# Kernel optimization log

Measured on AMD Instinct MI355X. Metric: run time of the kernel, lower is better.

## Reference

```python
import jax, jax.numpy as jnp
import numpy as np

D_MODEL = 256; N_HEADS = 8; N_LEVELS = 4; N_POINTS = 4; D_FFN = 1024
BS = 8; NQ = 100; NKPT = 17
LEVEL_SHAPES = [(160, 160), (80, 80), (40, 40), (20, 20)]  # (H, W) per level
LEN_V = sum(h * w for h, w in LEVEL_SHAPES)  # 34000


def layer_norm(x, g, b, eps=1e-5):
    m = x.mean(-1, keepdims=True)
    v = ((x - m) ** 2).mean(-1, keepdims=True)
    return (x - m) * jax.lax.rsqrt(v + eps) * g + b


def mha(q, k, v, Wqkv, bqkv, Wo, bo):
    # torch nn.MultiheadAttention, batch_first, eval mode (no dropout)
    d = q.shape[-1]; dh = d // N_HEADS
    def proj(x, W, b):
        return (x @ W.T + b).reshape(*x.shape[:-1], N_HEADS, dh)
    qp = proj(q, Wqkv[:d], bqkv[:d])
    kp = proj(k, Wqkv[d:2 * d], bqkv[d:2 * d])
    vp = proj(v, Wqkv[2 * d:], bqkv[2 * d:])
    att = jnp.einsum('bqhd,bkhd->bhqk', qp, kp) / jnp.sqrt(jnp.asarray(dh, q.dtype))
    att = jax.nn.softmax(att, -1)
    out = jnp.einsum('bhqk,bkhd->bqhd', att, vp).reshape(q.shape)
    return out @ Wo.T + bo


def bilinear_sample(val, loc, h, w):
    # val: (B, H, h*w, Dh); loc: (B, Lq, H, P, 2) normalized to [0,1]
    # matches F.grid_sample(align_corners=False, padding_mode='zeros') on grid 2*loc-1
    B, Lq, H, P, _ = loc.shape
    px = loc[..., 0] * w - 0.5
    py = loc[..., 1] * h - 0.5
    x0f = jnp.floor(px); y0f = jnp.floor(py)
    lx = px - x0f; ly = py - y0f
    x0 = x0f.astype(jnp.int32); y0 = y0f.astype(jnp.int32)
    out = jnp.zeros((B, H, Lq, P, val.shape[-1]), val.dtype)
    for dx, dy, wt in ((0, 0, (1 - lx) * (1 - ly)), (1, 0, lx * (1 - ly)),
                       (0, 1, (1 - lx) * ly), (1, 1, lx * ly)):
        xi = x0 + dx; yi = y0 + dy
        valid = ((xi >= 0) & (xi < w) & (yi >= 0) & (yi < h)).astype(val.dtype)
        idx = jnp.clip(yi, 0, h - 1) * w + jnp.clip(xi, 0, w - 1)  # (B,Lq,H,P)
        idx = idx.transpose(0, 2, 1, 3).reshape(B, H, Lq * P)
        g = jnp.take_along_axis(val, idx[..., None], axis=2).reshape(B, H, Lq, P, -1)
        out = out + g * (wt * valid).transpose(0, 2, 1, 3)[..., None]
    return out  # (B, H, Lq, P, Dh)


def ms_deform_attn(query, ref_points, memory, off_W, off_b, aw_W, aw_b,
                   val_W, val_b, outp_W, outp_b):
    B, Lq, _ = query.shape
    dh = D_MODEL // N_HEADS
    value = (memory @ val_W.T + val_b).reshape(B, LEN_V, N_HEADS, dh)
    off = (query @ off_W.T + off_b).reshape(B, Lq, N_HEADS, N_LEVELS, N_POINTS, 2)
    aw = (query @ aw_W.T + aw_b).reshape(B, Lq, N_HEADS, N_LEVELS * N_POINTS)
    aw = jax.nn.softmax(aw, -1).reshape(B, Lq, N_HEADS, N_LEVELS, N_POINTS)
    normalizer = jnp.array([[w, h] for h, w in LEVEL_SHAPES], dtype=query.dtype)  # (L,2) as (W,H)
    loc = ref_points[:, :, None, :, None, :] + off / normalizer[None, None, None, :, None, :]
    out = jnp.zeros((B, Lq, N_HEADS, dh), query.dtype)
    start = 0
    for l, (h, w) in enumerate(LEVEL_SHAPES):
        vl = value[:, start:start + h * w].transpose(0, 2, 1, 3)  # (B,H,hw,Dh)
        s = bilinear_sample(vl, loc[:, :, :, l], h, w)            # (B,H,Lq,P,Dh)
        out = out + jnp.einsum('bhqpd,bqhp->bqhd', s, aw[:, :, :, l])
        start += h * w
    return out.reshape(B, Lq, D_MODEL) @ outp_W.T + outp_b


def setup_inputs() -> dict:
    key = jax.random.key(0)
    ks = iter(jax.random.split(key, 40))
    d = D_MODEL
    def w(shape, s=0.02):
        return jax.random.normal(next(ks), shape, jnp.float32) * s
    inp = {
        'tgt_pose': jax.random.normal(next(ks), (BS, NQ, NKPT, d), jnp.float32),
        'tgt_pose_query_pos': jax.random.normal(next(ks), (BS, NQ, NKPT, d), jnp.float32),
        'tgt_pose_reference_points': jax.random.uniform(next(ks), (BS, NQ * NKPT, N_LEVELS, 2), jnp.float32),
        'memory': jax.random.normal(next(ks), (BS, LEN_V, d), jnp.float32),
        'win_Wqkv': w((3 * d, d)), 'win_bqkv': jnp.zeros((3 * d,), jnp.float32),
        'win_Wo': w((d, d)), 'win_bo': jnp.zeros((d,), jnp.float32),
        'win_ng': jnp.ones((d,), jnp.float32), 'win_nb': jnp.zeros((d,), jnp.float32),
        'acr_Wqkv': w((3 * d, d)), 'acr_bqkv': jnp.zeros((3 * d,), jnp.float32),
        'acr_Wo': w((d, d)), 'acr_bo': jnp.zeros((d,), jnp.float32),
        'acr_ng': jnp.ones((d,), jnp.float32), 'acr_nb': jnp.zeros((d,), jnp.float32),
        'off_W': w((N_HEADS * N_LEVELS * N_POINTS * 2, d)),
        'off_b': jax.random.uniform(next(ks), (N_HEADS * N_LEVELS * N_POINTS * 2,), jnp.float32, -1.0, 1.0),
        'aw_W': w((N_HEADS * N_LEVELS * N_POINTS, d)), 'aw_b': jnp.zeros((N_HEADS * N_LEVELS * N_POINTS,), jnp.float32),
        'val_W': w((d, d)), 'val_b': jnp.zeros((d,), jnp.float32),
        'outp_W': w((d, d)), 'outp_b': jnp.zeros((d,), jnp.float32),
        'gate_W': w((2 * d, 2 * d)), 'gate_b': jnp.zeros((2 * d,), jnp.float32),
        'gate_ng': jnp.ones((d,), jnp.float32), 'gate_nb': jnp.zeros((d,), jnp.float32),
        'ffn_W1': w((D_FFN, d)), 'ffn_b1': jnp.zeros((D_FFN,), jnp.float32),
        'ffn_W2': w((d, D_FFN)), 'ffn_b2': jnp.zeros((d,), jnp.float32),
        'n2_g': jnp.ones((d,), jnp.float32), 'n2_b': jnp.zeros((d,), jnp.float32),
        'memory_spatial_shapes': jnp.array(LEVEL_SHAPES, jnp.int32),
    }
    return inp


def reference(tgt_pose, tgt_pose_query_pos, tgt_pose_reference_points, memory,
              win_Wqkv, win_bqkv, win_Wo, win_bo, win_ng, win_nb,
              acr_Wqkv, acr_bqkv, acr_Wo, acr_bo, acr_ng, acr_nb,
              off_W, off_b, aw_W, aw_b, val_W, val_b, outp_W, outp_b,
              gate_W, gate_b, gate_ng, gate_nb,
              ffn_W1, ffn_b1, ffn_W2, ffn_b2, n2_g, n2_b,
              memory_spatial_shapes):
    bs, nq, K, d = tgt_pose.shape
    # with_pos_embed mutates tgt_pose in place in the torch code -> residual includes pos
    tgt = tgt_pose + tgt_pose_query_pos
    # within-attention over keypoints of each query
    x = tgt.reshape(bs * nq, K, d)
    t2 = mha(x, x, x, win_Wqkv, win_bqkv, win_Wo, win_bo).reshape(bs, nq, K, d)
    tgt = layer_norm(tgt + t2, win_ng, win_nb)
    # across-attention over queries for each keypoint
    xk = tgt.transpose(0, 2, 1, 3).reshape(bs * K, nq, d)
    t2 = mha(xk, xk, xk, acr_Wqkv, acr_bqkv, acr_Wo, acr_bo)
    tgt = layer_norm(xk + t2, acr_ng, acr_nb).reshape(bs, K, nq, d).transpose(0, 2, 1, 3)
    # second in-place pos add before deformable cross-attn (also feeds gateway)
    tgt_q = tgt + tgt_pose_query_pos
    t2 = ms_deform_attn(tgt_q.reshape(bs, nq * K, d), tgt_pose_reference_points, memory,
                        off_W, off_b, aw_W, aw_b, val_W, val_b, outp_W, outp_b)
    t2 = t2.reshape(bs, nq, K, d)
    # Gate
    g = jax.nn.sigmoid(jnp.concatenate([tgt_q, t2], -1) @ gate_W.T + gate_b)
    g1, g2 = jnp.split(g, 2, -1)
    tgt = layer_norm(g1 * tgt_q + g2 * t2, gate_ng, gate_nb)
    # FFN
    h = jax.nn.relu(tgt @ ffn_W1.T + ffn_b1)
    tgt = tgt + h @ ffn_W2.T + ffn_b2
    tgt = layer_norm(jnp.clip(tgt, -65504.0, 65504.0), n2_g, n2_b)
    return tgt
```

## Files before the change

### kernel.cpp

```cpp
#include <hip/hip_runtime.h>
#include <hip/hip_bf16.h>

#define NH 8
#define BS_ 8
#define NQ_ 100
#define NK_ 17
#define LQ 1700
#define T_TOK 13600
#define LEN_VV 34000

typedef __attribute__((ext_vector_type(8))) short short8v;
typedef __attribute__((ext_vector_type(8))) __bf16 bf16x8;
typedef __attribute__((ext_vector_type(4))) float f32x4;

__device__ __forceinline__ short f2bf(float f){
  __hip_bfloat16 h = __float2bfloat16(f);
  return *reinterpret_cast<short*>(&h);
}
__device__ __forceinline__ float bf2f(short s){
  return __uint_as_float(((uint)(unsigned short)s) << 16);
}
__device__ __forceinline__ short8v cvt8(float4 a, float4 b){
  short8v u;
  u[0]=f2bf(a.x); u[1]=f2bf(a.y); u[2]=f2bf(a.z); u[3]=f2bf(a.w);
  u[4]=f2bf(b.x); u[5]=f2bf(b.y); u[6]=f2bf(b.z); u[7]=f2bf(b.w);
  return u;
}

__global__ __launch_bounds__(256, 4) void mgemm_k(const float* __restrict__ A,
                                                  const float* __restrict__ W,
                                                  const float* __restrict__ bias,
                                                  __hip_bfloat16* __restrict__ Cb,
                                                  int M, int N, int K, int nbx){
  __shared__ short sh[128 * 136];
  short* As = sh;
  short* Ws = sh + 128 * 64;
  int total = gridDim.x;
  int q = total >> 3, r = total & 7;
  int x = blockIdx.x & 7, k = blockIdx.x >> 3;
  int j = (x < r) ? x * (q + 1) + k : r * (q + 1) + (x - r) * q + k;
  const int tid = threadIdx.x;
  const int bm = (j / nbx) * 128, bn = (j % nbx) * 128;
  const int wave = tid >> 6, lane = tid & 63;
  const int wm = (wave >> 1) * 64, wn = (wave & 1) * 64;
  const int s = tid & 7;
  const int row0 = tid >> 3;
  f32x4 acc[4][4] = {};
  const int lrow = lane & 15, lk = lane >> 4;

  for (int k0 = 0; k0 < K; k0 += 64){
#pragma unroll
    for (int i = 0; i < 4; i++){
      int row = row0 + i * 32;
      int gr = bm + row;
      int sw = ((s ^ (row & 7)) << 3) + row * 64;
      short8v va = {};
      if (gr < M){
        const float* p = A + (size_t)gr * K + k0 + s * 8;
        va = cvt8(((const float4*)p)[0], ((const float4*)p)[1]);
      }
      *(short8v*)&As[sw] = va;
      const float* q2 = W + (size_t)(bn + row) * K + k0 + s * 8;
      *(short8v*)&Ws[sw] = cvt8(((const float4*)q2)[0], ((const float4*)q2)[1]);
    }
    __syncthreads();
#pragma unroll
    for (int ks = 0; ks < 2; ks++){
      short8v af[4], bw[4];
      int slot = ks * 4 + lk;
#pragma unroll
      for (int m = 0; m < 4; m++){
        int rr = wm + m * 16 + lrow;
        af[m] = *(const short8v*)&As[rr * 64 + ((slot ^ (rr & 7)) << 3)];
      }
#pragma unroll
      for (int n = 0; n < 4; n++){
        int rr = wn + n * 16 + lrow;
        bw[n] = *(const short8v*)&Ws[rr * 64 + ((slot ^ (rr & 7)) << 3)];
      }
#pragma unroll
      for (int m = 0; m < 4; m++)
#pragma unroll
        for (int n = 0; n < 4; n++)
          acc[m][n] = __builtin_amdgcn_mfma_f32_16x16x32_bf16(
              __builtin_bit_cast(bf16x8, af[m]),
              __builtin_bit_cast(bf16x8, bw[n]), acc[m][n], 0, 0, 0);
    }
    __syncthreads();
  }
  const int STR = 136;
#pragma unroll
  for (int n = 0; n < 4; n++){
    int col = wn + n * 16 + lrow;
    float bsv = bias[bn + col];
#pragma unroll
    for (int m = 0; m < 4; m++){
#pragma unroll
      for (int i = 0; i < 4; i++){
        int row = wm + m * 16 + lk * 4 + i;
        sh[row * STR + col] = f2bf(acc[m][n][i] + bsv);
      }
    }
  }
  __syncthreads();
#pragma unroll
  for (int it = 0; it < 8; it++){
    int rr = it * 16 + (tid >> 4);
    int chunk = tid & 15;
    if (bm + rr < M){
      uint4 v = *(const uint4*)((const char*)sh + rr * 272 + chunk * 16);
      *(uint4*)((char*)Cb + ((size_t)(bm + rr) * N + bn) * 2 + chunk * 16) = v;
    }
  }
}

template<int EPI, int ADDA, int INB>
__global__ __launch_bounds__(256) void mgemmP_k(const void* __restrict__ Av,
                                                const float* __restrict__ A2,
                                                const float* __restrict__ W,
                                                const float* __restrict__ bias,
                                                __hip_bfloat16* __restrict__ Cb,
                                                int M, int N, int K, int nbx){
  __shared__ short sh[128 * 136];
  short* As = sh;
  short* Ws = sh + 128 * 64;
  const float* A = (const float*)Av;
  const short* Ab = (const short*)Av;
  const int tid = threadIdx.x;
  const int j = blockIdx.x;
  const int bm = (j / nbx) * 128, bn = (j % nbx) * 128;
  const int wave = tid >> 6, lane = tid & 63;
  const int wm = (wave >> 1) * 64, wn = (wave & 1) * 64;
  const int s = tid & 7;
  const int row0 = tid >> 3;
  f32x4 acc[4][4] = {};
  const int lrow = lane & 15, lk = lane >> 4;

  float4 ra[INB ? 1 : 8], rw[8];
  short8v rab[INB ? 4 : 1];
#pragma unroll
  for (int i = 0; i < 4; i++){
    int row = row0 + i * 32;
    int gr = bm + row;
    if (INB){
      short8v z = {};
      rab[INB ? i : 0] = (gr < M) ? *(const short8v*)(Ab + (size_t)gr * K + s * 8) : z;
    } else {
      float4 z = make_float4(0.f, 0.f, 0.f, 0.f);
      if (gr < M){
        const float* p = A + (size_t)gr * K + s * 8;
        float4 x0 = ((const float4*)p)[0], x1 = ((const float4*)p)[1];
        if (ADDA){
          const float* q2 = A2 + (size_t)gr * K + s * 8;
          float4 y0 = ((const float4*)q2)[0], y1 = ((const float4*)q2)[1];
          x0.x+=y0.x; x0.y+=y0.y; x0.z+=y0.z; x0.w+=y0.w;
          x1.x+=y1.x; x1.y+=y1.y; x1.z+=y1.z; x1.w+=y1.w;
        }
        ra[INB ? 0 : (2 * i)] = x0; ra[INB ? 0 : (2 * i + 1)] = x1;
      } else { ra[INB ? 0 : (2 * i)] = z; ra[INB ? 0 : (2 * i + 1)] = z; }
    }
    const float* q = W + (size_t)(bn + row) * K + s * 8;
    rw[2 * i] = ((const float4*)q)[0]; rw[2 * i + 1] = ((const float4*)q)[1];
  }

  for (int k0 = 0; k0 < K; k0 += 64){
#pragma unroll
    for (int i = 0; i < 4; i++){
      int row = row0 + i * 32;
      int sw = ((s ^ (row & 7)) << 3) + row * 64;
      if (INB) *(short8v*)&As[sw] = rab[INB ? i : 0];
      else     *(short8v*)&As[sw] = cvt8(ra[INB ? 0 : (2 * i)], ra[INB ? 0 : (2 * i + 1)]);
      *(short8v*)&Ws[sw] = cvt8(rw[2 * i], rw[2 * i + 1]);
    }
    __syncthreads();
    if (k0 + 64 < K){
#pragma unroll
      for (int i = 0; i < 4; i++){
        int row = row0 + i * 32;
        int gr = bm + row;
        if (INB){
          short8v z = {};
          rab[INB ? i : 0] = (gr < M) ? *(const short8v*)(Ab + (size_t)gr * K + k0 + 64 + s * 8) : z;
        } else {
          float4 z = make_float4(0.f, 0.f, 0.f, 0.f);
          if (gr < M){
            const float* p = A + (size_t)gr * K + k0 + 64 + s * 8;
            float4 x0 = ((const float4*)p)[0], x1 = ((const float4*)p)[1];
            if (ADDA){
              const float* q2 = A2 + (size_t)gr * K + k0 + 64 + s * 8;
              float4 y0 = ((const float4*)q2)[0], y1 = ((const float4*)q2)[1];
              x0.x+=y0.x; x0.y+=y0.y; x0.z+=y0.z; x0.w+=y0.w;
              x1.x+=y1.x; x1.y+=y1.y; x1.z+=y1.z; x1.w+=y1.w;
            }
            ra[INB ? 0 : (2 * i)] = x0; ra[INB ? 0 : (2 * i + 1)] = x1;
          } else { ra[INB ? 0 : (2 * i)] = z; ra[INB ? 0 : (2 * i + 1)] = z; }
        }
        const float* q = W + (size_t)(bn + row) * K + k0 + 64 + s * 8;
        rw[2 * i] = ((const float4*)q)[0]; rw[2 * i + 1] = ((const float4*)q)[1];
      }
    }
#pragma unroll
    for (int ks = 0; ks < 2; ks++){
      short8v af[4], bw[4];
      int slot = ks * 4 + lk;
#pragma unroll
      for (int m = 0; m < 4; m++){
        int rr = wm + m * 16 + lrow;
        af[m] = *(const short8v*)&As[rr * 64 + ((slot ^ (rr & 7)) << 3)];
      }
#pragma unroll
      for (int n = 0; n < 4; n++){
        int rr = wn + n * 16 + lrow;
        bw[n] = *(const short8v*)&Ws[rr * 64 + ((slot ^ (rr & 7)) << 3)];
      }
#pragma unroll
      for (int m = 0; m < 4; m++)
#pragma unroll
        for (int n = 0; n < 4; n++)
          acc[m][n] = __builtin_amdgcn_mfma_f32_16x16x32_bf16(
              __builtin_bit_cast(bf16x8, af[m]),
              __builtin_bit_cast(bf16x8, bw[n]), acc[m][n], 0, 0, 0);
    }
    __syncthreads();
  }
  const int STR = 136;
#pragma unroll
  for (int n = 0; n < 4; n++){
    int col = wn + n * 16 + lrow;
    float bsv = bias[bn + col];
#pragma unroll
    for (int m = 0; m < 4; m++){
#pragma unroll
      for (int i = 0; i < 4; i++){
        int row = wm + m * 16 + lk * 4 + i;
        float c = acc[m][n][i] + bsv;
        if (EPI == 1) c = fmaxf(c, 0.f);
        sh[row * STR + col] = f2bf(c);
      }
    }
  }
  __syncthreads();
#pragma unroll
  for (int it = 0; it < 8; it++){
    int rr = it * 16 + (tid >> 4);
    int chunk = tid & 15;
    if (bm + rr < M){
      uint4 v = *(const uint4*)((const char*)sh + rr * 272 + chunk * 16);
      *(uint4*)((char*)Cb + ((size_t)(bm + rr) * N + bn) * 2 + chunk * 16) = v;
    }
  }
}

template<int SITE, int OUTB>
__global__ __launch_bounds__(256) void gln_k(const short* __restrict__ Abf,
                                             const float* __restrict__ W,
                                             const float* __restrict__ bias,
                                             const float* __restrict__ r0,
                                             const float* __restrict__ r1,
                                             const float* __restrict__ g,
                                             const float* __restrict__ be,
                                             void* __restrict__ outv,
                                             int M, int K){
  __shared__ short As[32 * 64];
  __shared__ short Ws[256 * 64];
  __shared__ float part[32][4][2];
  __shared__ float stats[32][2];
  const int tid = threadIdx.x;
  const int bm = blockIdx.x * 32;
  const int wave = tid >> 6, lane = tid & 63;
  const int wn = wave * 64;
  const int s = tid & 7, row0 = tid >> 3;
  const int lrow = lane & 15, lk = lane >> 4;
  f32x4 acc[2][4] = {};

  short8v pa = {};
  { int gr = bm + row0; if (gr < M) pa = *(const short8v*)(Abf + (size_t)gr * K + s * 8); }
  short8v pwb[8];
#pragma unroll
  for (int i = 0; i < 8; i++){
    const float* wp = W + (size_t)(row0 + i * 32) * K + s * 8;
    pwb[i] = cvt8(((const float4*)wp)[0], ((const float4*)wp)[1]);
  }

  for (int k0 = 0; k0 < K; k0 += 64){
    *(short8v*)&As[row0 * 64 + ((s ^ (row0 & 7)) << 3)] = pa;
#pragma unroll
    for (int i = 0; i < 8; i++){
      int row = row0 + i * 32;
      *(short8v*)&Ws[row * 64 + ((s ^ (row & 7)) << 3)] = pwb[i];
    }
    __syncthreads();
    if (k0 + 64 < K){
      int gr = bm + row0;
      pa = (short8v){};
      if (gr < M) pa = *(const short8v*)(Abf + (size_t)gr * K + k0 + 64 + s * 8);
#pragma unroll
      for (int i = 0; i < 8; i++){
        const float* wp = W + (size_t)(row0 + i * 32) * K + k0 + 64 + s * 8;
        pwb[i] = cvt8(((const float4*)wp)[0], ((const float4*)wp)[1]);
      }
    }
#pragma unroll
    for (int ks = 0; ks < 2; ks++){
      int slot = ks * 4 + lk;
      short8v af[2], bw[4];
#pragma unroll
      for (int m = 0; m < 2; m++){
        int rr = m * 16 + lrow;
        af[m] = *(const short8v*)&As[rr * 64 + ((slot ^ (rr & 7)) << 3)];
      }
#pragma unroll
      for (int n = 0; n < 4; n++){
        int rr = wn + n * 16 + lrow;
        bw[n] = *(const short8v*)&Ws[rr * 64 + ((slot ^ (rr & 7)) << 3)];
      }
#pragma unroll
      for (int m = 0; m < 2; m++)
#pragma unroll
        for (int n = 0; n < 4; n++)
          acc[m][n] = __builtin_amdgcn_mfma_f32_16x16x32_bf16(
              __builtin_bit_cast(bf16x8, af[m]),
              __builtin_bit_cast(bf16x8, bw[n]), acc[m][n], 0, 0, 0);
    }
    __syncthreads();
  }

#pragma unroll
  for (int m = 0; m < 2; m++){
#pragma unroll
    for (int i = 0; i < 4; i++){
      int row = m * 16 + lk * 4 + i;
      int grow = bm + row;
      float s1 = 0.f, s2 = 0.f;
      if (grow < M){
#pragma unroll
        for (int n = 0; n < 4; n++){
          int col = wn + n * 16 + lrow;
          float x = acc[m][n][i] + bias[col] + r0[(size_t)grow * 256 + col];
          if (SITE == 0) x += r1[(size_t)grow * 256 + col];
          if (SITE == 2) x = fminf(fmaxf(x, -65504.f), 65504.f);
          acc[m][n][i] = x;
          s1 += x; s2 += x * x;
        }
      }
#pragma unroll
      for (int msk = 1; msk <= 8; msk <<= 1){
        s1 += __shfl_xor(s1, msk, 64);
        s2 += __shfl_xor(s2, msk, 64);
      }
      if (lrow == 0){ part[row][wave][0] = s1; part[row][wave][1] = s2; }
    }
  }
  __syncthreads();
  if (tid < 32){
    float s1 = part[tid][0][0] + part[tid][1][0] + part[tid][2][0] + part[tid][3][0];
    float s2 = part[tid][0][1] + part[tid][1][1] + part[tid][2][1] + part[tid][3][1];
    float mean = s1 * (1.f / 256.f);
    float var = s2 * (1.f / 256.f) - mean * mean;
    stats[tid][0] = mean;
    stats[tid][1] = rsqrtf(fmaxf(var, 0.f) + 1e-5f);
  }
  __syncthreads();
#pragma unroll
  for (int m = 0; m < 2; m++){
#pragma unroll
    for (int i = 0; i < 4; i++){
      int row = m * 16 + lk * 4 + i;
      int grow = bm + row;
      if (grow >= M) continue;
      float mean = stats[row][0], rstd = stats[row][1];
      size_t orow = grow;
      if (SITE == 0){
        int bi = grow / LQ; int rem = grow % LQ; int qq = rem / NK_; int kk = rem % NK_;
        orow = (size_t)bi * LQ + kk * NQ_ + qq;
      }
#pragma unroll
      for (int n = 0; n < 4; n++){
        int col = wn + n * 16 + lrow;
        float o = (acc[m][n][i] - mean) * rstd * g[col] + be[col];
        if (OUTB) ((short*)outv)[orow * 256 + col] = f2bf(o);
        else      ((float*)outv)[orow * 256 + col] = o;
      }
    }
  }
}

__global__ __launch_bounds__(256) void glnoa_k(const short* __restrict__ Abf,
                                               const float* __restrict__ W,
                                               const float* __restrict__ bias,
                                               const short* __restrict__ r0b,
                                               const float* __restrict__ qpos,
                                               const float* __restrict__ g,
                                               const float* __restrict__ be,
                                               short* __restrict__ TQout,
                                               float* __restrict__ OFFAW,
                                               const float* __restrict__ off_W,
                                               const float* __restrict__ aw_W,
                                               const float* __restrict__ off_b,
                                               const float* __restrict__ aw_b,
                                               int M){
  __shared__ short smem[32 * 256 + 384 * 64];
  __shared__ float part[32][4][2];
  __shared__ float stats[32][2];
  short* As1 = smem;
  short* Ws1 = smem + 32 * 64;
  short* As2 = smem;
  short* Ws2 = smem + 32 * 256;
  const int K = 256;
  const int tid = threadIdx.x;
  const int bm = blockIdx.x * 32;
  const int wave = tid >> 6, lane = tid & 63;
  const int wn = wave * 64;
  const int s = tid & 7, row0 = tid >> 3;
  const int lrow = lane & 15, lk = lane >> 4;
  f32x4 acc[2][4] = {};

  short8v pa = {};
  { int gr = bm + row0; if (gr < M) pa = *(const short8v*)(Abf + (size_t)gr * K + s * 8); }
  short8v pwb[8];
#pragma unroll
  for (int i = 0; i < 8; i++){
    const float* wp = W + (size_t)(row0 + i * 32) * K + s * 8;
    pwb[i] = cvt8(((const float4*)wp)[0], ((const float4*)wp)[1]);
  }
  for (int k0 = 0; k0 < K; k0 += 64){
    *(short8v*)&As1[row0 * 64 + ((s ^ (row0 & 7)) << 3)] = pa;
#pragma unroll
    for (int i = 0; i < 8; i++){
      int row = row0 + i * 32;
      *(short8v*)&Ws1[row * 64 + ((s ^ (row & 7)) << 3)] = pwb[i];
    }
    __syncthreads();
    if (k0 + 64 < K){
      int gr = bm + row0;
      pa = (short8v){};
      if (gr < M) pa = *(const short8v*)(Abf + (size_t)gr * K + k0 + 64 + s * 8);
#pragma unroll
      for (int i = 0; i < 8; i++){
        const float* wp = W + (size_t)(row0 + i * 32) * K + k0 + 64 + s * 8;
        pwb[i] = cvt8(((const float4*)wp)[0], ((const float4*)wp)[1]);
      }
    }
#pragma unroll
    for (int ks = 0; ks < 2; ks++){
      int slot = ks * 4 + lk;
      short8v af[2], bw[4];
#pragma unroll
      for (int m = 0; m < 2; m++){
        int rr = m * 16 + lrow;
        af[m] = *(const short8v*)&As1[rr * 64 + ((slot ^ (rr & 7)) << 3)];
      }
#pragma unroll
      for (int n = 0; n < 4; n++){
        int rr = wn + n * 16 + lrow;
        bw[n] = *(const short8v*)&Ws1[rr * 64 + ((slot ^ (rr & 7)) << 3)];
      }
#pragma unroll
      for (int m = 0; m < 2; m++)
#pragma unroll
        for (int n = 0; n < 4; n++)
          acc[m][n] = __builtin_amdgcn_mfma_f32_16x16x32_bf16(
              __builtin_bit_cast(bf16x8, af[m]),
              __builtin_bit_cast(bf16x8, bw[n]), acc[m][n], 0, 0, 0);
    }
    __syncthreads();
  }
#pragma unroll
  for (int m = 0; m < 2; m++){
#pragma unroll
    for (int i = 0; i < 4; i++){
      int row = m * 16 + lk * 4 + i;
      int grow = bm + row;
      float s1 = 0.f, s2 = 0.f;
      if (grow < M){
#pragma unroll
        for (int n = 0; n < 4; n++){
          int col = wn + n * 16 + lrow;
          float x = acc[m][n][i] + bias[col] + bf2f(r0b[(size_t)grow * 256 + col]);
          acc[m][n][i] = x;
          s1 += x; s2 += x * x;
        }
      }
#pragma unroll
      for (int msk = 1; msk <= 8; msk <<= 1){
        s1 += __shfl_xor(s1, msk, 64);
        s2 += __shfl_xor(s2, msk, 64);
      }
      if (lrow == 0){ part[row][wave][0] = s1; part[row][wave][1] = s2; }
    }
  }
  __syncthreads();
  if (tid < 32){
    float s1 = part[tid][0][0] + part[tid][1][0] + part[tid][2][0] + part[tid][3][0];
    float s2 = part[tid][0][1] + part[tid][1][1] + part[tid][2][1] + part[tid][3][1];
    float mean = s1 * (1.f / 256.f);
    float var = s2 * (1.f / 256.f) - mean * mean;
    stats[tid][0] = mean;
    stats[tid][1] = rsqrtf(fmaxf(var, 0.f) + 1e-5f);
  }
  __syncthreads();
#pragma unroll
  for (int m = 0; m < 2; m++){
#pragma unroll
    for (int i = 0; i < 4; i++){
      int row = m * 16 + lk * 4 + i;
      int grow = bm + row;
      float mean = stats[row][0], rstd = stats[row][1];
      size_t orow = 0;
      if (grow < M){
        int bi = grow / LQ; int rem = grow % LQ; int kk = rem / NQ_; int qq = rem % NQ_;
        orow = (size_t)bi * LQ + qq * NK_ + kk;
      }
#pragma unroll
      for (int n = 0; n < 4; n++){
        int col = wn + n * 16 + lrow;
        float tq = 0.f;
        if (grow < M){
          float o = (acc[m][n][i] - mean) * rstd * g[col] + be[col];
          tq = o + qpos[orow * 256 + col];
          TQout[orow * 256 + col] = f2bf(tq);
        }
        As2[row * 256 + ((((col >> 3) ^ (row & 7)) << 3) + (col & 7))] = f2bf(tq);
      }
    }
  }
  __syncthreads();
  const int wn2 = wave * 96;
  f32x4 acc2[2][6] = {};
  for (int k0 = 0; k0 < 256; k0 += 64){
#pragma unroll
    for (int it = 0; it < 12; it++){
      int wr = row0 + it * 32;
      const float* Wp = (wr < 256) ? off_W + (size_t)wr * 256 + k0
                                   : aw_W + (size_t)(wr - 256) * 256 + k0;
      *(short8v*)&Ws2[wr * 64 + ((s ^ (wr & 7)) << 3)] =
          cvt8(((const float4*)(Wp + s * 8))[0], ((const float4*)(Wp + s * 8))[1]);
    }
    __syncthreads();
#pragma unroll
    for (int ks = 0; ks < 2; ks++){
      int slotl = ks * 4 + lk;
      int slotg = (k0 >> 3) + slotl;
      short8v af[2], bw[6];
#pragma unroll
      for (int m = 0; m < 2; m++){
        int rr = m * 16 + lrow;
        af[m] = *(const short8v*)&As2[rr * 256 + ((slotg ^ (rr & 7)) << 3)];
      }
#pragma unroll
      for (int n = 0; n < 6; n++){
        int rr = wn2 + n * 16 + lrow;
        bw[n] = *(const short8v*)&Ws2[rr * 64 + ((slotl ^ (rr & 7)) << 3)];
      }
#pragma unroll
      for (int m = 0; m < 2; m++)
#pragma unroll
        for (int n = 0; n < 6; n++)
          acc2[m][n] = __builtin_amdgcn_mfma_f32_16x16x32_bf16(
              __builtin_bit_cast(bf16x8, af[m]),
              __builtin_bit_cast(bf16x8, bw[n]), acc2[m][n], 0, 0, 0);
    }
    __syncthreads();
  }
#pragma unroll
  for (int m = 0; m < 2; m++){
#pragma unroll
    for (int i = 0; i < 4; i++){
      int row = m * 16 + lk * 4 + i;
      int grow = bm + row;
      if (grow >= M) continue;
      int bi = grow / LQ; int rem = grow % LQ; int kk = rem / NQ_; int qq = rem % NQ_;
      size_t orow = (size_t)bi * LQ + qq * NK_ + kk;
#pragma unroll
      for (int n = 0; n < 6; n++){
        int col = wn2 + n * 16 + lrow;
        float c = acc2[m][n][i] + ((col < 256) ? off_b[col] : aw_b[col - 256]);
        OFFAW[orow * 384 + col] = c;
      }
    }
  }
}

__global__ __launch_bounds__(256) void t2gateln_k(const short* __restrict__ ABF,
                                                  const float* __restrict__ outp_W,
                                                  const float* __restrict__ outp_b,
                                                  const short* __restrict__ TQ,
                                                  const float* __restrict__ gW,
                                                  const float* __restrict__ gbias,
                                                  const float* __restrict__ g,
                                                  const float* __restrict__ be,
                                                  float* __restrict__ out, int M){
  __shared__ short As[32 * 64];
  __shared__ short T2s[32 * 256];
  __shared__ short Ws[512 * 64];
  const int tid = threadIdx.x;
  const int bm = blockIdx.x * 32;
  const int wave = tid >> 6, lane = tid & 63;
  const int s = tid & 7, row0 = tid >> 3;
  const int lrow = lane & 15, lk = lane >> 4;

  {
    const int wn = wave * 64;
    f32x4 acc[2][4] = {};
    for (int k0 = 0; k0 < 256; k0 += 64){
      {
        short8v v = {};
        int gr = bm + row0;
        if (gr < M) v = *(const short8v*)(ABF + (size_t)gr * 256 + k0 + s * 8);
        *(short8v*)&As[row0 * 64 + ((s ^ (row0 & 7)) << 3)] = v;
      }
#pragma unroll
      for (int i = 0; i < 8; i++){
        int row = row0 + i * 32;
        const float* wp = outp_W + (size_t)row * 256 + k0 + s * 8;
        *(short8v*)&Ws[row * 64 + ((s ^ (row & 7)) << 3)] =
            cvt8(((const float4*)wp)[0], ((const float4*)wp)[1]);
      }
      __syncthreads();
#pragma unroll
      for (int ks = 0; ks < 2; ks++){
        int slot = ks * 4 + lk;
        short8v af[2], bw[4];
#pragma unroll
        for (int m = 0; m < 2; m++){
          int rr = m * 16 + lrow;
          af[m] = *(const short8v*)&As[rr * 64 + ((slot ^ (rr & 7)) << 3)];
        }
#pragma unroll
        for (int n = 0; n < 4; n++){
          int rr = wn + n * 16 + lrow;
          bw[n] = *(const short8v*)&Ws[rr * 64 + ((slot ^ (rr & 7)) << 3)];
        }
#pragma unroll
        for (int m = 0; m < 2; m++)
#pragma unroll
          for (int n = 0; n < 4; n++)
            acc[m][n] = __builtin_amdgcn_mfma_f32_16x16x32_bf16(
                __builtin_bit_cast(bf16x8, af[m]),
                __builtin_bit_cast(bf16x8, bw[n]), acc[m][n], 0, 0, 0);
      }
      __syncthreads();
    }
#pragma unroll
    for (int m = 0; m < 2; m++){
#pragma unroll
      for (int i = 0; i < 4; i++){
        int row = m * 16 + lk * 4 + i;
#pragma unroll
        for (int n = 0; n < 4; n++){
          int col = wn + n * 16 + lrow;
          float t2v = acc[m][n][i] + outp_b[col];
          T2s[row * 256 + ((((col >> 3) ^ (row & 7)) << 3) + (col & 7))] = f2bf(t2v);
        }
      }
    }
  }
  __syncthreads();

  const int wn = wave * 128;
  f32x4 acc[2][8] = {};
  for (int kt = 0; kt < 8; kt++){
    int k0 = kt * 64;
    if (kt < 4){
      short8v v = {};
      int gr = bm + row0;
      if (gr < M) v = *(const short8v*)(TQ + (size_t)gr * 256 + k0 + s * 8);
      *(short8v*)&As[row0 * 64 + ((s ^ (row0 & 7)) << 3)] = v;
    }
#pragma unroll
    for (int i = 0; i < 16; i++){
      int row = row0 + i * 32;
      const float* wp = gW + (size_t)row * 512 + k0 + s * 8;
      *(short8v*)&Ws[row * 64 + ((s ^ (row & 7)) << 3)] =
          cvt8(((const float4*)wp)[0], ((const float4*)wp)[1]);
    }
    __syncthreads();
#pragma unroll
    for (int ks = 0; ks < 2; ks++){
      int slot = ks * 4 + lk;
      short8v af[2], bw[8];
#pragma unroll
      for (int m = 0; m < 2; m++){
        int rr = m * 16 + lrow;
        if (kt < 4){
          af[m] = *(const short8v*)&As[rr * 64 + ((slot ^ (rr & 7)) << 3)];
        } else {
          int slotg = ((k0 - 256) >> 3) + slot;
          af[m] = *(const short8v*)&T2s[rr * 256 + ((slotg ^ (rr & 7)) << 3)];
        }
      }
#pragma unroll
      for (int n = 0; n < 8; n++){
        int rr = wn + n * 16 + lrow;
        bw[n] = *(const short8v*)&Ws[rr * 64 + ((slot ^ (rr & 7)) << 3)];
      }
#pragma unroll
      for (int m = 0; m < 2; m++)
#pragma unroll
        for (int n = 0; n < 8; n++)
          acc[m][n] = __builtin_amdgcn_mfma_f32_16x16x32_bf16(
              __builtin_bit_cast(bf16x8, af[m]),
              __builtin_bit_cast(bf16x8, bw[n]), acc[m][n], 0, 0, 0);
    }
    __syncthreads();
  }
  short* gb = Ws;
  const int GSTR = 520;
#pragma unroll
  for (int n = 0; n < 8; n++){
    int col = wn + n * 16 + lrow;
    float bsv = gbias[col];
#pragma unroll
    for (int m = 0; m < 2; m++){
#pragma unroll
      for (int i = 0; i < 4; i++){
        int row = m * 16 + lk * 4 + i;
        float c = acc[m][n][i] + bsv;
        gb[row * GSTR + col] = f2bf(1.f / (1.f + __expf(-c)));
      }
    }
  }
  __syncthreads();
  {
    int row = tid >> 3, cg = tid & 7;
    int grow = bm + row;
    float x[32];
    float s1 = 0.f, s2 = 0.f;
    if (grow < M){
#pragma unroll
      for (int jv = 0; jv < 4; jv++){
        int c0 = cg * 32 + jv * 8;
        short8v aqv = *(const short8v*)(TQ + (size_t)grow * 256 + c0);
        int slot2 = (cg * 4 + jv) ^ (row & 7);
        const short* t2p = &T2s[row * 256 + slot2 * 8];
#pragma unroll
        for (int jj = 0; jj < 8; jj++){
          float g1 = bf2f(gb[row * GSTR + c0 + jj]);
          float g2 = bf2f(gb[row * GSTR + 256 + c0 + jj]);
          float xv = g1 * bf2f(aqv[jj]) + g2 * bf2f(t2p[jj]);
          x[jv * 8 + jj] = xv; s1 += xv; s2 += xv * xv;
        }
      }
    }
    s1 += __shfl_xor(s1, 1, 64); s2 += __shfl_xor(s2, 1, 64);
    s1 += __shfl_xor(s1, 2, 64); s2 += __shfl_xor(s2, 2, 64);
    s1 += __shfl_xor(s1, 4, 64); s2 += __shfl_xor(s2, 4, 64);
    float mean = s1 * (1.f / 256.f);
    float var = s2 * (1.f / 256.f) - mean * mean;
    float rstd = rsqrtf(fmaxf(var, 0.f) + 1e-5f);
    if (grow < M){
#pragma unroll
      for (int jv = 0; jv < 4; jv++){
        int c0 = cg * 32 + jv * 8;
        float4 o0, o1;
#pragma unroll
        for (int jj = 0; jj < 8; jj++){
          int c = c0 + jj;
          float o = (x[jv * 8 + jj] - mean) * rstd * g[c] + be[c];
          if (jj < 4) ((float*)&o0)[jj] = o; else ((float*)&o1)[jj - 4] = o;
        }
        *(float4*)(out + (size_t)grow * 256 + c0) = o0;
        *(float4*)(out + (size_t)grow * 256 + c0 + 4) = o1;
      }
    }
  }
}

template<int TP, int NSPL>
__global__ __launch_bounds__(256) void mha_mfma_k(const short* __restrict__ qkv,
                                                  __hip_bfloat16* __restrict__ out, int S){
  constexpr int MT = TP / 16;
  constexpr int KSTEPS = (TP + 31) / 32;
  constexpr int KS32 = KSTEPS * 32;
  constexpr int VSTRB = (KS32 == 128) ? 256 : 128;
  constexpr int CH = (MT + NSPL - 1) / NSPL;
  __shared__ short QK[2][TP][64];
  __shared__ short Vt[2][32][VSTRB / 2];
  __shared__ float Sc[2][16][128];
  __shared__ float rinv[2][16];

  const int tid = threadIdx.x;
  const int bid = blockIdx.x;
  const int batch = bid / (4 * NSPL);
  const int rem = bid % (4 * NSPL);
  const int hp = rem / NSPL;
  const int half = rem % NSPL;
  const int mtlo = half * CH;
  const int mthi = (mtlo + CH < MT) ? (mtlo + CH) : MT;
  const int wave = tid >> 6, lane = tid & 63;
  const int hh = wave >> 1, wsub = wave & 1;
  const int lrow = lane & 15, lk = lane >> 4;
  const float scale = 0.17677669529663687f;
  const size_t qbase = (size_t)batch * S * 768;

  for (int idx = tid; idx < 2 * TP * 4; idx += 256){
    int h2 = idx >= TP * 4;
    int rm = idx - h2 * TP * 4;
    int j = rm >> 2, s = rm & 3;
    int h = hp * 2 + h2;
    short8v qv = {}, kv = {};
    if (j < S){
      const short* p = qkv + qbase + (size_t)j * 768 + h * 32 + s * 8;
      qv = *(const short8v*)p;
      kv = *(const short8v*)(p + 256);
    }
    *(short8v*)&QK[h2][j][(s ^ (j & 7)) << 3] = qv;
    *(short8v*)&QK[h2][j][((s + 4) ^ (j & 7)) << 3] = kv;
  }
  for (int idx = tid; idx < 2 * KS32 * 4; idx += 256){
    int h2 = idx >= KS32 * 4;
    int rm = idx - h2 * KS32 * 4;
    int j = rm >> 2, e8 = rm & 3;
    int h = hp * 2 + h2;
    short8v v = {};
    if (j < S) v = *(const short8v*)(qkv + qbase + (size_t)j * 768 + h * 32 + 512 + e8 * 8);
#pragma unroll
    for (int c = 0; c < 8; c++){
      int e = e8 * 8 + c;
      char* pb = (char*)&Vt[h2][0][0] + e * VSTRB + (((j >> 3) ^ (e & 7)) << 4) + ((j & 7) << 1);
      *(short*)pb = v[c];
    }
  }
  __syncthreads();

  for (int mt = mtlo; mt < mthi; mt++){
    for (int nt = wsub; nt < MT; nt += 2){
      int ar = mt * 16 + lrow;
      short8v aq = *(const short8v*)&QK[hh][ar][(lk ^ (ar & 7)) << 3];
      int br = nt * 16 + lrow;
      short8v bk = *(const short8v*)&QK[hh][br][((lk + 4) ^ (br & 7)) << 3];
      f32x4 z = {};
      f32x4 d = __builtin_amdgcn_mfma_f32_16x16x32_bf16(
          __builtin_bit_cast(bf16x8, aq), __builtin_bit_cast(bf16x8, bk), z, 0, 0, 0);
#pragma unroll
      for (int i = 0; i < 4; i++){
        int rr = lk * 4 + i;
        int c = nt * 16 + lrow;
        Sc[hh][rr][(((c >> 2) ^ (rr & 7)) << 2) + (c & 3)] = d[i] * scale;
      }
    }
    __syncthreads();
    if (wsub == 0){
      int rr = lane >> 2, p = lane & 3;
      int grow = mt * 16 + rr;
      int Seff = (grow < S) ? S : 0;
      float mx = -1e30f;
#pragma unroll
      for (int m = 0; m < KSTEPS; m++){
        int j = p + 4 * m;
#pragma unroll
        for (int hf = 0; hf < 2; hf++){
          int ls = 2 * j + hf;
          float4 v = *(const float4*)&Sc[hh][rr][(ls ^ (rr & 7)) << 2];
          int c0 = ls * 4;
          mx = fmaxf(mx, (c0 + 0 < Seff) ? v.x : -1e30f);
          mx = fmaxf(mx, (c0 + 1 < Seff) ? v.y : -1e30f);
          mx = fmaxf(mx, (c0 + 2 < Seff) ? v.z : -1e30f);
          mx = fmaxf(mx, (c0 + 3 < Seff) ? v.w : -1e30f);
        }
      }
      mx = fmaxf(mx, __shfl_xor(mx, 1, 64));
      mx = fmaxf(mx, __shfl_xor(mx, 2, 64));
      float sum = 0.f;
#pragma unroll
      for (int m = 0; m < KSTEPS; m++){
        int j = p + 4 * m;
        float ev[8];
#pragma unroll
        for (int hf = 0; hf < 2; hf++){
          int ls = 2 * j + hf;
          float4 v = *(const float4*)&Sc[hh][rr][(ls ^ (rr & 7)) << 2];
          int c0 = ls * 4;
          ev[hf * 4 + 0] = (c0 + 0 < Seff) ? __expf(v.x - mx) : 0.f;
          ev[hf * 4 + 1] = (c0 + 1 < Seff) ? __expf(v.y - mx) : 0.f;
          ev[hf * 4 + 2] = (c0 + 2 < Seff) ? __expf(v.z - mx) : 0.f;
          ev[hf * 4 + 3] = (c0 + 3 < Seff) ? __expf(v.w - mx) : 0.f;
        }
        short8v pb;
#pragma unroll
        for (int q2 = 0; q2 < 8; q2++){ pb[q2] = f2bf(ev[q2]); sum += ev[q2]; }
        *(short8v*)((char*)&Sc[hh][rr][0] + ((j ^ (rr & 7)) << 4)) = pb;
      }
      sum += __shfl_xor(sum, 1, 64);
      sum += __shfl_xor(sum, 2, 64);
      if (p == 0) rinv[hh][rr] = (sum > 0.f) ? 1.f / sum : 0.f;
    }
    __syncthreads();
    {
      int nt2 = wsub;
      f32x4 acc = {};
#pragma unroll
      for (int ks = 0; ks < KSTEPS; ks++){
        int slot = ks * 4 + lk;
        short8v ap = *(const short8v*)((const char*)&Sc[hh][lrow][0] + ((slot ^ (lrow & 7)) << 4));
        int e = nt2 * 16 + lrow;
        short8v bv = *(const short8v*)((const char*)&Vt[hh][0][0] + e * VSTRB + ((slot ^ (e & 7)) << 4));
        acc = __builtin_amdgcn_mfma_f32_16x16x32_bf16(
            __builtin_bit_cast(bf16x8, ap), __builtin_bit_cast(bf16x8, bv), acc, 0, 0, 0);
      }
      int h = hp * 2 + hh;
#pragma unroll
      for (int i = 0; i < 4; i++){
        int row = mt * 16 + lk * 4 + i;
        if (row < S){
          float rv = rinv[hh][lk * 4 + i];
          out[((size_t)batch * S + row) * 256 + h * 32 + nt2 * 16 + lrow] =
              __float2bfloat16(acc[i] * rv);
        }
      }
    }
    __syncthreads();
  }
}

__global__ __launch_bounds__(256) void deform_k(const __hip_bfloat16* __restrict__ val,
                                                const float* __restrict__ offaw,
                                                const float* __restrict__ ref,
                                                unsigned int* __restrict__ outb){
  __shared__ uint2 meta[32][16][4];
  const int tid = threadIdx.x;
  const int t0 = blockIdx.x * 4;
  {
    int g = tid >> 3;
    int pair = tid & 7;
    int lt = g >> 3, h = g & 7;
    int t = t0 + lt;
    int b = t / LQ;
    int p0 = pair * 2;
    int l = p0 >> 2;
    const int starts[4] = {0, 25600, 32000, 33600};
    const int HS[4] = {160, 80, 40, 20};
    int w = HS[l];
    const float* ap = offaw + (size_t)t * 384 + 256 + h * 16;
    float a0 = ap[p0];
    float a1 = ap[p0 + 1];
    float mx = fmaxf(a0, a1);
#pragma unroll
    for (int m = 1; m <= 4; m <<= 1) mx = fmaxf(mx, __shfl_xor(mx, m, 64));
    float e0 = expf(a0 - mx), e1 = expf(a1 - mx);
    float s = e0 + e1;
#pragma unroll
    for (int m = 1; m <= 4; m <<= 1) s += __shfl_xor(s, m, 64);
    float inv = 1.f / s;
    float rx = ref[((size_t)t * 4 + l) * 2 + 0];
    float ry = ref[((size_t)t * 4 + l) * 2 + 1];
    float4 ov = *(const float4*)(offaw + (size_t)t * 384 + h * 32 + l * 8 + p0 * 2);
    int vbase = (b * LEN_VV + starts[l]) * 128 + h * 16;
#pragma unroll
    for (int pp = 0; pp < 2; pp++){
      float wgt = (pp ? e1 : e0) * inv;
      float px = rx * w + (pp ? ov.z : ov.x) - 0.5f;
      float py = ry * w + (pp ? ov.w : ov.y) - 0.5f;
      float x0f = floorf(px), y0f = floorf(py);
      float lx = px - x0f, ly = py - y0f;
      int x0 = (int)x0f, y0 = (int)y0f;
#pragma unroll
      for (int c = 0; c < 4; c++){
        int dx = c & 1, dy = c >> 1;
        int xi = x0 + dx, yi = y0 + dy;
        bool ok = (xi >= 0) & (xi < w) & (yi >= 0) & (yi < w);
        float cw = ok ? wgt * (dx ? lx : 1.f - lx) * (dy ? ly : 1.f - ly) : 0.f;
        uint idx = ok ? (uint)(vbase + (yi * w + xi) * 128) : 0u;
        uint2 m2; m2.x = idx; m2.y = __float_as_uint(cw);
        meta[g][p0 + pp][c] = m2;
      }
    }
  }
  __syncthreads();
  const uint2* V2 = (const uint2*)val;
  int sg = tid >> 3, lane8 = tid & 7;
  int lt = sg >> 3, h = sg & 7;
  int t = t0 + lt;
  float a0 = 0.f, a1 = 0.f, a2 = 0.f, a3 = 0.f;
#pragma unroll 4
  for (int c = 0; c < 64; c++){
    uint2 mw = meta[sg][c >> 2][c & 3];
    float wv = __uint_as_float(mw.y);
    uint2 v = V2[(size_t)(mw.x >> 1) + lane8];
    a0 += wv * __uint_as_float(v.x << 16);
    a1 += wv * __uint_as_float(v.x & 0xffff0000u);
    a2 += wv * __uint_as_float(v.y << 16);
    a3 += wv * __uint_as_float(v.y & 0xffff0000u);
  }
  uint2 u;
  u.x = ((uint)(unsigned short)f2bf(a1) << 16) | (uint)(unsigned short)f2bf(a0);
  u.y = ((uint)(unsigned short)f2bf(a3) << 16) | (uint)(unsigned short)f2bf(a2);
  ((uint2*)outb)[((size_t)t * 256 + h * 32) / 4 + lane8] = u;
}

extern "C" void kernel_launch(void* const* d_in, const int* in_sizes, int n_in,
                              void* d_out, int out_size, void* d_ws, size_t ws_size,
                              hipStream_t stream){
  const float* tgt_pose = (const float*)d_in[0];
  const float* qpos     = (const float*)d_in[1];
  const float* refp     = (const float*)d_in[2];
  const float* memory   = (const float*)d_in[3];
  const float* win_Wqkv = (const float*)d_in[4];
  const float* win_bqkv = (const float*)d_in[5];
  const float* win_Wo   = (const float*)d_in[6];
  const float* win_bo   = (const float*)d_in[7];
  const float* win_ng   = (const float*)d_in[8];
  const float* win_nb   = (const float*)d_in[9];
  const float* acr_Wqkv = (const float*)d_in[10];
  const float* acr_bqkv = (const float*)d_in[11];
  const float* acr_Wo   = (const float*)d_in[12];
  const float* acr_bo   = (const float*)d_in[13];
  const float* acr_ng   = (const float*)d_in[14];
  const float* acr_nb   = (const float*)d_in[15];
  const float* off_W    = (const float*)d_in[16];
  const float* off_b    = (const float*)d_in[17];
  const float* aw_W     = (const float*)d_in[18];
  const float* aw_b     = (const float*)d_in[19];
  const float* val_W    = (const float*)d_in[20];
  const float* val_b    = (const float*)d_in[21];
  const float* outp_W   = (const float*)d_in[22];
  const float* outp_b   = (const float*)d_in[23];
  const float* gate_W   = (const float*)d_in[24];
  const float* gate_b   = (const float*)d_in[25];
  const float* gate_ng  = (const float*)d_in[26];
  const float* gate_nb  = (const float*)d_in[27];
  const float* ffn_W1   = (const float*)d_in[28];
  const float* ffn_b1   = (const float*)d_in[29];
  const float* ffn_W2   = (const float*)d_in[30];
  const float* ffn_b2   = (const float*)d_in[31];
  const float* n2_g     = (const float*)d_in[32];
  const float* n2_b     = (const float*)d_in[33];

  float* out = (float*)d_out;
  char* ws = (char*)d_ws;
  const size_t TB = (size_t)T_TOK * 256 * 4;
  float* B2 = (float*)(ws);
  char* p = ws + TB;
  short* B1b = (short*)p;  p += (size_t)T_TOK * 256 * 2;
  short* Qb  = (short*)p;  p += (size_t)T_TOK * 768 * 2;
  short* ABF = (short*)p;  p += (size_t)T_TOK * 256 * 2;
  short* TQb = (short*)p;  p += (size_t)T_TOK * 256 * 2;
  float* OFFAW = (float*)p; p += (size_t)T_TOK * 384 * 4;
  char* Vregion = p;
  __hip_bfloat16* V = (__hip_bfloat16*)Vregion;
  short* FF = (short*)Vregion;

  const int GM128 = (T_TOK + 127) / 128;
  const int GM32  = (T_TOK + 31) / 32;

  mgemm_k<<<2 * 2125, 256, 0, stream>>>(memory, val_W, val_b, V, BS_ * LEN_VV, 256, 256, 2);
  mgemmP_k<0,1,0><<<6 * GM128, 256, 0, stream>>>(tgt_pose, qpos, win_Wqkv, win_bqkv, (__hip_bfloat16*)Qb, T_TOK, 768, 256, 6);
  mha_mfma_k<32,1><<<800 * 4, 256, 0, stream>>>(Qb, (__hip_bfloat16*)ABF, 17);
  gln_k<0,1><<<GM32, 256, 0, stream>>>(ABF, win_Wo, win_bo, tgt_pose, qpos, win_ng, win_nb, B1b, T_TOK, 256);
  mgemmP_k<0,0,1><<<6 * GM128, 256, 0, stream>>>(B1b, nullptr, acr_Wqkv, acr_bqkv, (__hip_bfloat16*)Qb, T_TOK, 768, 256, 6);
  mha_mfma_k<112,2><<<136 * 8, 256, 0, stream>>>(Qb, (__hip_bfloat16*)ABF, 100);
  glnoa_k<<<GM32, 256, 0, stream>>>(ABF, acr_Wo, acr_bo, B1b, qpos, acr_ng, acr_nb,
                                    TQb, OFFAW, off_W, aw_W, off_b, aw_b, T_TOK);
  deform_k<<<T_TOK / 4, 256, 0, stream>>>(V, OFFAW, refp, (unsigned int*)ABF);
  t2gateln_k<<<GM32, 256, 0, stream>>>(ABF, outp_W, outp_b, TQb, gate_W, gate_b,
                                       gate_ng, gate_nb, B2, T_TOK);
  mgemmP_k<1,0,0><<<8 * GM128, 256, 0, stream>>>(B2, nullptr, ffn_W1, ffn_b1, (__hip_bfloat16*)FF, T_TOK, 1024, 256, 8);
  gln_k<2,0><<<GM32, 256, 0, stream>>>(FF, ffn_W2, ffn_b2, B2, nullptr, n2_g, n2_b, out, T_TOK, 1024);
}
```

Baseline: 477.8 us.

## Split fused output-proj/gate kernel into separate 64x64 GEMM and gate-LN kernels

The fused t2gateln kernel, which computed the deformable-attention output projection in shared memory before the gate GEMM and layernorm, is split in two. A new generic 64x64-tile bf16 MFMA GEMM kernel writes the projected t2 to a new bf16 workspace buffer, and a slimmer gate+layernorm kernel reads TQ and T2 from global memory. The fused kernel used a lot of LDS per block, which limits occupancy; the split lowers that footprint and gives the projection a better-shaped grid. The cost is an extra launch plus a global write and read of the t2 intermediate.

Result: faster. 462.7 us (-3.2%).

```diff
diff --git a/kernel.cpp b/kernel.cpp
--- a/kernel.cpp
+++ b/kernel.cpp
@@ -247,6 +247,129 @@
     if (bm + rr < M){
       uint4 v = *(const uint4*)((const char*)sh + rr * 272 + chunk * 16);
       *(uint4*)((char*)Cb + ((size_t)(bm + rr) * N + bn) * 2 + chunk * 16) = v;
+    }
+  }
+}
+
+template<int EPI, int OUTB, int INB, int DUALA>
+__global__ __launch_bounds__(256) void g64_k(const void* __restrict__ Av,
+                                             const void* __restrict__ A1v,
+                                             const float* __restrict__ W0,
+                                             const float* __restrict__ W1,
+                                             int NSPLIT,
+                                             const float* __restrict__ bias0,
+                                             const float* __restrict__ bias1,
+                                             const float* __restrict__ RES,
+                                             float* __restrict__ Cf,
+                                             __hip_bfloat16* __restrict__ Cb,
+                                             int M, int N, int K, int sA){
+  __shared__ short sh64[2 * 64 * 64];
+  short* As = sh64;
+  short* Ws = sh64 + 64 * 64;
+  const int tid = threadIdx.x;
+  const int bn = blockIdx.x * 64, bm = blockIdx.y * 64;
+  const int wave = tid >> 6, lane = tid & 63;
+  const int wm = (wave >> 1) * 32, wn = (wave & 1) * 32;
+  const int s = tid & 7, row0 = tid >> 3;
+  const int lrow = lane & 15, lk = lane >> 4;
+  f32x4 acc[2][2] = {};
+
+  for (int k0 = 0; k0 < K; k0 += 64){
+#pragma unroll
+    for (int i = 0; i < 2; i++){
+      int row = row0 + i * 32;
+      int sw = ((s ^ (row & 7)) << 3) + row * 64;
+      short8v v = {};
+      int gr = bm + row;
+      if (gr < M){
+        if (INB){
+          v = *(const short8v*)((const short*)Av + (size_t)gr * sA + k0 + s * 8);
+        } else {
+          const float* Ap;
+          if (DUALA) Ap = (k0 < 256) ? (const float*)Av + (size_t)gr * 256 + k0
+                                     : (const float*)A1v + (size_t)gr * 256 + (k0 - 256);
+          else Ap = (const float*)Av + (size_t)gr * sA + k0;
+          v = cvt8(((const float4*)(Ap + s * 8))[0], ((const float4*)(Ap + s * 8))[1]);
+        }
+      }
+      *(short8v*)&As[sw] = v;
+      int wr = bn + row;
+      const float* Wp = (wr < NSPLIT) ? W0 + (size_t)wr * K + k0
+                                      : W1 + (size_t)(wr - NSPLIT) * K + k0;
+      *(short8v*)&Ws[sw] = cvt8(((const float4*)(Wp + s * 8))[0], ((const float4*)(Wp + s * 8))[1]);
+    }
+    __syncthreads();
+#pragma unroll
+    for (int ks = 0; ks < 2; ks++){
+      int slot = ks * 4 + lk;
+      short8v af[2], bw[2];
+#pragma unroll
+      for (int m = 0; m < 2; m++){
+        int rr = wm + m * 16 + lrow;
+        af[m] = *(const short8v*)&As[rr * 64 + ((slot ^ (rr & 7)) << 3)];
+      }
+#pragma unroll
+      for (int n = 0; n < 2; n++){
+        int rr = wn + n * 16 + lrow;
+        bw[n] = *(const short8v*)&Ws[rr * 64 + ((slot ^ (rr & 7)) << 3)];
+      }
+#pragma unroll
+      for (int m = 0; m < 2; m++)
+#pragma unroll
+        for (int n = 0; n < 2; n++)
+          acc[m][n] = __builtin_amdgcn_mfma_f32_16x16x32_bf16(
+              __builtin_bit_cast(bf16x8, af[m]),
+              __builtin_bit_cast(bf16x8, bw[n]), acc[m][n], 0, 0, 0);
+    }
+    __syncthreads();
+  }
+  if (OUTB){
+    const int STR = 72;
+#pragma unroll
+    for (int n = 0; n < 2; n++){
+      int col = wn + n * 16 + lrow;
+      int gc = bn + col;
+      float bsv = (gc < NSPLIT) ? bias0[gc] : bias1[gc - NSPLIT];
+#pragma unroll
+      for (int m = 0; m < 2; m++){
+#pragma unroll
+        for (int i = 0; i < 4; i++){
+          int row = wm + m * 16 + lk * 4 + i;
+          float c = acc[m][n][i] + bsv;
+          if (EPI == 1) c = fmaxf(c, 0.f);
+          if (EPI == 2) c = 1.f / (1.f + expf(-c));
+          sh64[row * STR + col] = f2bf(c);
+        }
+      }
+    }
+    __syncthreads();
+#pragma unroll
+    for (int it = 0; it < 2; it++){
+      int rr = it * 32 + (tid >> 3);
+      int chunk = tid & 7;
+      if (bm + rr < M){
+        uint4 v = *(const uint4*)((const char*)sh64 + rr * 144 + chunk * 16);
+        *(uint4*)((char*)Cb + ((size_t)(bm + rr) * N + bn) * 2 + chunk * 16) = v;
+      }
+    }
+  } else {
+#pragma unroll
+    for (int n = 0; n < 2; n++){
+      int gc = bn + wn + n * 16 + lrow;
+      float bsv = (gc < NSPLIT) ? bias0[gc] : bias1[gc - NSPLIT];
+#pragma unroll
+      for (int m = 0; m < 2; m++){
+#pragma unroll
+        for (int i = 0; i < 4; i++){
+          int row = bm + wm + m * 16 + lk * 4 + i;
+          if (row >= M) continue;
+          float c = acc[m][n][i] + bsv;
+          if (EPI == 1) c = fmaxf(c, 0.f);
+          if (EPI == 2) c = 1.f / (1.f + expf(-c));
+          if (EPI == 3) c += RES[(size_t)row * N + gc];
+          Cf[(size_t)row * N + gc] = c;
+        }
+      }
     }
   }
 }
@@ -581,96 +704,38 @@
   }
 }
 
-__global__ __launch_bounds__(256) void t2gateln_k(const short* __restrict__ ABF,
-                                                  const float* __restrict__ outp_W,
-                                                  const float* __restrict__ outp_b,
-                                                  const short* __restrict__ TQ,
-                                                  const float* __restrict__ gW,
-                                                  const float* __restrict__ gbias,
-                                                  const float* __restrict__ g,
-                                                  const float* __restrict__ be,
-                                                  float* __restrict__ out, int M){
-  __shared__ short As[32 * 64];
-  __shared__ short T2s[32 * 256];
-  __shared__ short Ws[512 * 64];
+__global__ __launch_bounds__(256) void gateln_k(const short* __restrict__ TQ,
+                                                const short* __restrict__ T2,
+                                                const float* __restrict__ W,
+                                                const float* __restrict__ bias,
+                                                const float* __restrict__ g,
+                                                const float* __restrict__ be,
+                                                float* __restrict__ out, int M){
+  __shared__ short sh[32 * 64 + 512 * 64];
+  short* As = sh;
+  short* Ws = sh + 32 * 64;
   const int tid = threadIdx.x;
   const int bm = blockIdx.x * 32;
   const int wave = tid >> 6, lane = tid & 63;
+  const int wn = wave * 128;
   const int s = tid & 7, row0 = tid >> 3;
   const int lrow = lane & 15, lk = lane >> 4;
-
-  {
-    const int wn = wave * 64;
-    f32x4 acc[2][4] = {};
-    for (int k0 = 0; k0 < 256; k0 += 64){
-      {
-        short8v v = {};
-        int gr = bm + row0;
-        if (gr < M) v = *(const short8v*)(ABF + (size_t)gr * 256 + k0 + s * 8);
-        *(short8v*)&As[row0 * 64 + ((s ^ (row0 & 7)) << 3)] = v;
-      }
-#pragma unroll
-      for (int i = 0; i < 8; i++){
-        int row = row0 + i * 32;
-        const float* wp = outp_W + (size_t)row * 256 + k0 + s * 8;
-        *(short8v*)&Ws[row * 64 + ((s ^ (row & 7)) << 3)] =
-            cvt8(((const float4*)wp)[0], ((const float4*)wp)[1]);
-      }
-      __syncthreads();
-#pragma unroll
-      for (int ks = 0; ks < 2; ks++){
-        int slot = ks * 4 + lk;
-        short8v af[2], bw[4];
-#pragma unroll
-        for (int m = 0; m < 2; m++){
-          int rr = m * 16 + lrow;
-          af[m] = *(const short8v*)&As[rr * 64 + ((slot ^ (rr & 7)) << 3)];
-        }
-#pragma unroll
-        for (int n = 0; n < 4; n++){
-          int rr = wn + n * 16 + lrow;
-          bw[n] = *(const short8v*)&Ws[rr * 64 + ((slot ^ (rr & 7)) << 3)];
-        }
-#pragma unroll
-        for (int m = 0; m < 2; m++)
-#pragma unroll
-          for (int n = 0; n < 4; n++)
-            acc[m][n] = __builtin_amdgcn_mfma_f32_16x16x32_bf16(
-                __builtin_bit_cast(bf16x8, af[m]),
-                __builtin_bit_cast(bf16x8, bw[n]), acc[m][n], 0, 0, 0);
-      }
-      __syncthreads();
-    }
-#pragma unroll
-    for (int m = 0; m < 2; m++){
-#pragma unroll
-      for (int i = 0; i < 4; i++){
-        int row = m * 16 + lk * 4 + i;
-#pragma unroll
-        for (int n = 0; n < 4; n++){
-          int col = wn + n * 16 + lrow;
-          float t2v = acc[m][n][i] + outp_b[col];
-          T2s[row * 256 + ((((col >> 3) ^ (row & 7)) << 3) + (col & 7))] = f2bf(t2v);
-        }
-      }
-    }
-  }
-  __syncthreads();
-
-  const int wn = wave * 128;
   f32x4 acc[2][8] = {};
-  for (int kt = 0; kt < 8; kt++){
-    int k0 = kt * 64;
-    if (kt < 4){
+
+  for (int k0 = 0; k0 < 512; k0 += 64){
+    {
       short8v v = {};
       int gr = bm + row0;
-      if (gr < M) v = *(const short8v*)(TQ + (size_t)gr * 256 + k0 + s * 8);
+      if (gr < M){
+        v = (k0 < 256) ? *(const short8v*)(TQ + (size_t)gr * 256 + k0 + s * 8)
+                       : *(const short8v*)(T2 + (size_t)gr * 256 + (k0 - 256) + s * 8);
+      }
       *(short8v*)&As[row0 * 64 + ((s ^ (row0 & 7)) << 3)] = v;
     }
 #pragma unroll
     for (int i = 0; i < 16; i++){
       int row = row0 + i * 32;
-      const float* wp = gW + (size_t)row * 512 + k0 + s * 8;
+      const float* wp = W + (size_t)row * 512 + k0 + s * 8;
       *(short8v*)&Ws[row * 64 + ((s ^ (row & 7)) << 3)] =
           cvt8(((const float4*)wp)[0], ((const float4*)wp)[1]);
     }
@@ -682,12 +747,7 @@
 #pragma unroll
       for (int m = 0; m < 2; m++){
         int rr = m * 16 + lrow;
-        if (kt < 4){
-          af[m] = *(const short8v*)&As[rr * 64 + ((slot ^ (rr & 7)) << 3)];
-        } else {
-          int slotg = ((k0 - 256) >> 3) + slot;
-          af[m] = *(const short8v*)&T2s[rr * 256 + ((slotg ^ (rr & 7)) << 3)];
-        }
+        af[m] = *(const short8v*)&As[rr * 64 + ((slot ^ (rr & 7)) << 3)];
       }
 #pragma unroll
       for (int n = 0; n < 8; n++){
@@ -704,12 +764,12 @@
     }
     __syncthreads();
   }
-  short* gb = Ws;
+  short* gb = sh;
   const int GSTR = 520;
 #pragma unroll
   for (int n = 0; n < 8; n++){
     int col = wn + n * 16 + lrow;
-    float bsv = gbias[col];
+    float bsv = bias[col];
 #pragma unroll
     for (int m = 0; m < 2; m++){
 #pragma unroll
@@ -731,13 +791,12 @@
       for (int jv = 0; jv < 4; jv++){
         int c0 = cg * 32 + jv * 8;
         short8v aqv = *(const short8v*)(TQ + (size_t)grow * 256 + c0);
-        int slot2 = (cg * 4 + jv) ^ (row & 7);
-        const short* t2p = &T2s[row * 256 + slot2 * 8];
+        short8v t2v = *(const short8v*)(T2 + (size_t)grow * 256 + c0);
 #pragma unroll
         for (int jj = 0; jj < 8; jj++){
           float g1 = bf2f(gb[row * GSTR + c0 + jj]);
           float g2 = bf2f(gb[row * GSTR + 256 + c0 + jj]);
-          float xv = g1 * bf2f(aqv[jj]) + g2 * bf2f(t2p[jj]);
+          float xv = g1 * bf2f(aqv[jj]) + g2 * bf2f(t2v[jj]);
           x[jv * 8 + jj] = xv; s1 += xv; s2 += xv * xv;
         }
       }
@@ -1035,13 +1094,16 @@
   short* Qb  = (short*)p;  p += (size_t)T_TOK * 768 * 2;
   short* ABF = (short*)p;  p += (size_t)T_TOK * 256 * 2;
   short* TQb = (short*)p;  p += (size_t)T_TOK * 256 * 2;
+  short* T2b = (short*)p;  p += (size_t)T_TOK * 256 * 2;
   float* OFFAW = (float*)p; p += (size_t)T_TOK * 384 * 4;
   char* Vregion = p;
   __hip_bfloat16* V = (__hip_bfloat16*)Vregion;
   short* FF = (short*)Vregion;
 
   const int GM128 = (T_TOK + 127) / 128;
+  const int GM64  = (T_TOK + 63) / 64;
   const int GM32  = (T_TOK + 31) / 32;
+  const int BIG = 1 << 30;
 
   mgemm_k<<<2 * 2125, 256, 0, stream>>>(memory, val_W, val_b, V, BS_ * LEN_VV, 256, 256, 2);
   mgemmP_k<0,1,0><<<6 * GM128, 256, 0, stream>>>(tgt_pose, qpos, win_Wqkv, win_bqkv, (__hip_bfloat16*)Qb, T_TOK, 768, 256, 6);
@@ -1052,8 +1114,8 @@
   glnoa_k<<<GM32, 256, 0, stream>>>(ABF, acr_Wo, acr_bo, B1b, qpos, acr_ng, acr_nb,
                                     TQb, OFFAW, off_W, aw_W, off_b, aw_b, T_TOK);
   deform_k<<<T_TOK / 4, 256, 0, stream>>>(V, OFFAW, refp, (unsigned int*)ABF);
-  t2gateln_k<<<GM32, 256, 0, stream>>>(ABF, outp_W, outp_b, TQb, gate_W, gate_b,
-                                       gate_ng, gate_nb, B2, T_TOK);
+  g64_k<0,1,1,0><<<dim3(4, GM64), 256, 0, stream>>>(ABF, nullptr, outp_W, outp_W, BIG, outp_b, outp_b, nullptr, nullptr, (__hip_bfloat16*)T2b, T_TOK, 256, 256, 256);
+  gateln_k<<<GM32, 256, 0, stream>>>(TQb, T2b, gate_W, gate_b, gate_ng, gate_nb, B2, T_TOK);
   mgemmP_k<1,0,0><<<8 * GM128, 256, 0, stream>>>(B2, nullptr, ffn_W1, ffn_b1, (__hip_bfloat16*)FF, T_TOK, 1024, 256, 8);
   gln_k<2,0><<<GM32, 256, 0, stream>>>(FF, ffn_W2, ffn_b2, B2, nullptr, n2_g, n2_b, out, T_TOK, 1024);
 }
```
